# Kernel optimization log

Hardware: AMD Instinct MI355X
Metric: run time of the kernel (lower is better)

Reference implementation:

```python
import jax, jax.numpy as jnp
import numpy as np

B, Q, K, D, U = 8, 128, 512, 256, 256  # batch, q_len, kv_len, feat dim, units
NEG_INF = -1e6


def setup_inputs() -> dict:
    key = jax.random.key(0)
    ks = jax.random.split(key, 7)
    query = jax.random.normal(ks[0], (B, Q, D), dtype=jnp.float32)
    k_in = jax.random.normal(ks[1], (B, K, D), dtype=jnp.float32)
    value = jax.random.normal(ks[2], (B, K, D), dtype=jnp.float32)
    valid_len = jax.random.randint(ks[3], (B,), 1, K + 1, dtype=jnp.int32)
    s = 1.0 / np.sqrt(D)
    Wq = jax.random.uniform(ks[4], (D, U), jnp.float32, -s, s)
    Wk = jax.random.uniform(ks[5], (D, U), jnp.float32, -s, s)
    v_w = jax.random.uniform(ks[6], (U,), jnp.float32, -1.0 / np.sqrt(U), 1.0 / np.sqrt(U))
    return {"query": query, "key": k_in, "value": value, "valid_len": valid_len,
            "Wq": Wq, "Wk": Wk, "v_w": v_w}


def reference(query, key, value, valid_len, Wq, Wk, v_w):
    # projections: [B,Q,U] and [B,K,U]
    q = jnp.einsum('bqd,du->bqu', query, Wq)
    k = jnp.einsum('bkd,du->bku', key, Wk)
    # additive features [B,Q,K,U] -> tanh -> reduce with v: scores [B,Q,K]
    feats = jnp.tanh(q[:, :, None, :] + k[:, None, :, :])
    scores = jnp.einsum('bqku,u->bqk', feats, v_w)
    # masked softmax over keys: positions >= valid_len[b] masked out
    mask = jnp.arange(K)[None, None, :] < valid_len[:, None, None]
    scores = jnp.where(mask, scores, NEG_INF)
    attn = jax.nn.softmax(scores, axis=-1)
    # dropout p=0.0 (eval) -> identity
    return jnp.einsum('bqk,bkd->bqd', attn, value)
```

## Files before the change

### kernel.cpp

```cpp
#include <hip/hip_runtime.h>
#include <hip/hip_fp16.h>

#ifndef __has_builtin
#define __has_builtin(x) 0
#endif

__device__ __forceinline__ float fast_exp2(float x) {
#if __has_builtin(__builtin_amdgcn_exp2f)
  return __builtin_amdgcn_exp2f(x);
#else
  return exp2f(x);
#endif
}
__device__ __forceinline__ float fast_rcp(float x) {
#if __has_builtin(__builtin_amdgcn_rcpf)
  return __builtin_amdgcn_rcpf(x);
#else
  return 1.0f / x;
#endif
}

constexpr int Bsz = 8, QL = 128, KL = 512, DD = 256, UU = 256;
constexpr float NEG_INF = -1e6f;
constexpr float C2 = 2.885390081777927f;

typedef __attribute__((ext_vector_type(8))) short bf16x8;
typedef __attribute__((ext_vector_type(4))) float f32x4;

__device__ __forceinline__ ushort f2bf(float x) {
  uint u = __float_as_uint(x);
  u += 0x7FFFu + ((u >> 16) & 1u);
  return (ushort)(u >> 16);
}
__device__ __forceinline__ float bf2f(ushort h) {
  return __uint_as_float(((uint)h) << 16);
}

__device__ ushort g_wpk[2][2][16][8][64][8];

__global__ __launch_bounds__(256) void wpack_kernel(
    const float* __restrict__ Wq, const float* __restrict__ Wk)
{
  const int tid = blockIdx.x * 256 + threadIdx.x;
  const int src = tid >> 13;
  const int ut  = (tid >> 9) & 15;
  const int ks  = (tid >> 6) & 7;
  const int l   = tid & 63;
  const int u   = ut * 16 + (l & 15);
  const int d0  = ks * 32 + (l >> 4) * 8;
  const float* __restrict__ W = src ? Wk : Wq;

  ushort hi[8], lo[8];
#pragma unroll
  for (int j = 0; j < 8; ++j) {
    const float x = W[(size_t)(d0 + j) * UU + u];
    const ushort h = f2bf(x);
    hi[j] = h;
    lo[j] = f2bf(x - bf2f(h));
  }
#pragma unroll
  for (int j = 0; j < 8; ++j) g_wpk[src][0][ut][ks][l][j] = hi[j];
#pragma unroll
  for (int j = 0; j < 8; ++j) g_wpk[src][1][ut][ks][l][j] = lo[j];
}

__global__ __launch_bounds__(256) void proj_mfma_kernel(
    const float* __restrict__ query, const float* __restrict__ key,
    const int* __restrict__ valid_len,
    float* __restrict__ qp, __half* __restrict__ kpT)
{
  const int t = threadIdx.x, w = t >> 6, l = t & 63;
  const int blk = blockIdx.x;
  const bool isQ = blk < 64;

  int b = 0, k0 = 0, row_mem;
  if (isQ) {
    row_mem = blk * 16;
  } else {
    const int kt = blk - 64;
    b  = kt >> 5;
    k0 = (kt & 31) * 16;
    if (k0 >= valid_len[b]) return;
    row_mem = b * KL + k0;
  }
  const float* __restrict__ in = isQ ? query : key;
  const int src = isQ ? 0 : 1;

  bf16x8 Ah[8], Al[8];
  {
    const float* __restrict__ arow =
        in + (size_t)(row_mem + (l & 15)) * DD + ((l >> 4) * 8);
#pragma unroll
    for (int s = 0; s < 8; ++s) {
      const float4 x0 = *reinterpret_cast<const float4*>(arow + s * 32);
      const float4 x1 = *reinterpret_cast<const float4*>(arow + s * 32 + 4);
      const float v[8] = {x0.x, x0.y, x0.z, x0.w, x1.x, x1.y, x1.z, x1.w};
#pragma unroll
      for (int j = 0; j < 8; ++j) {
        const ushort h = f2bf(v[j]);
        Ah[s][j] = (short)h;
        Al[s][j] = (short)f2bf(v[j] - bf2f(h));
      }
    }
  }

  const int ut0 = w * 4;
#pragma unroll
  for (int tt = 0; tt < 4; ++tt) {
    const int ut = ut0 + tt;
    f32x4 acc = {0.f, 0.f, 0.f, 0.f};
#pragma unroll
    for (int s = 0; s < 8; ++s) {
      const bf16x8 bh = *reinterpret_cast<const bf16x8*>(&g_wpk[src][0][ut][s][l][0]);
      const bf16x8 bl = *reinterpret_cast<const bf16x8*>(&g_wpk[src][1][ut][s][l][0]);
      acc = __builtin_amdgcn_mfma_f32_16x16x32_bf16(Ah[s], bh, acc, 0, 0, 0);
      acc = __builtin_amdgcn_mfma_f32_16x16x32_bf16(Al[s], bh, acc, 0, 0, 0);
      acc = __builtin_amdgcn_mfma_f32_16x16x32_bf16(Ah[s], bl, acc, 0, 0, 0);
    }
    const int u  = ut * 16 + (l & 15);
    const int r4 = (l >> 4) * 4;
    if (isQ) {
      float* __restrict__ o = qp + (size_t)(row_mem + r4) * UU + u;
      o[0]          = fast_exp2(C2 * acc[0]);
      o[UU]         = fast_exp2(C2 * acc[1]);
      o[2 * UU]     = fast_exp2(C2 * acc[2]);
      o[3 * UU]     = fast_exp2(C2 * acc[3]);
    } else {
      ushort4 v;
      v.x = __half_as_ushort(__float2half_rn(fast_exp2(C2 * acc[0])));
      v.y = __half_as_ushort(__float2half_rn(fast_exp2(C2 * acc[1])));
      v.z = __half_as_ushort(__float2half_rn(fast_exp2(C2 * acc[2])));
      v.w = __half_as_ushort(__float2half_rn(fast_exp2(C2 * acc[3])));
      *reinterpret_cast<ushort4*>(
          kpT + ((size_t)(b * UU) + u) * KL + k0 + r4) = v;
    }
  }
}

__global__ __launch_bounds__(512) void fused_attn_kernel(
    const float* __restrict__ value, const int* __restrict__ valid_len,
    const float* __restrict__ v_w, const float* __restrict__ qp,
    const __half* __restrict__ kpT, float* __restrict__ out)
{
  __shared__ __align__(16) float4 qpack[UU];
  __shared__ __align__(16) float2 sp_part[8][8][64];
  __shared__ __align__(16) float  sps0[KL];
  __shared__ __align__(16) float  sps1[KL];
  __shared__ __align__(16) float2 opart[DD];
  __shared__ float2 redM[8], redS[8];

  const int t = threadIdx.x;
  const int w = t >> 6, l = t & 63;

  const int g = blockIdx.x;
  const int x = g & 7;
  const int i = g >> 3;
  int vl[8];
#pragma unroll
  for (int bi = 0; bi < 8; ++bi) vl[bi] = valid_len[bi];
  const int rk = (i < 32) ? x : (7 - x);
  int b = 0;
#pragma unroll
  for (int bi = 0; bi < 8; ++bi) {
    int r = 0;
#pragma unroll
    for (int bj = 0; bj < 8; ++bj)
      r += (vl[bj] > vl[bi]) || (vl[bj] == vl[bi] && bj < bi);
    if (r == rk) b = bi;
  }
  const int vlen = vl[b];
  const int q0 = i * 2;
  const int nc = (vlen + 63) >> 6;

  if (t < UU) {
    qpack[t] = make_float4(qp[(size_t)(b * QL + q0) * UU + t],
                           qp[(size_t)(b * QL + q0 + 1) * UU + t],
                           v_w[t], 0.f);
  }
  __syncthreads();

  {
    const __half* __restrict__ kbase =
        kpT + ((size_t)(b * UU) + 32 * w) * KL + l;
    for (int c = 0; c < nc; ++c) {
      const int k64 = 64 * c;
      float a0 = 0.f, a1 = 0.f;
      float cb[8], nb[8];
#pragma unroll
      for (int j = 0; j < 8; ++j)
        cb[j] = __half2float(kbase[(size_t)j * KL + k64]);
#pragma unroll 1
      for (int ug = 0; ug < 32; ug += 8) {
        const int un = (ug + 8 < 32) ? ug + 8 : 0;
#pragma unroll
        for (int j = 0; j < 8; ++j)
          nb[j] = __half2float(kbase[(size_t)(un + j) * KL + k64]);
#pragma unroll
        for (int j = 0; j < 8; j += 2) {
          const float4 qv0 = qpack[32 * w + ug + j];
          const float4 qv1 = qpack[32 * w + ug + j + 1];
          const float d00 = fmaf(qv0.x, cb[j],     1.0f);
          const float d01 = fmaf(qv1.x, cb[j + 1], 1.0f);
          const float num0 = fmaf(qv0.z, d01, qv1.z * d00);
          a0 = fmaf(num0, fast_rcp(d00 * d01), a0);
          const float d10 = fmaf(qv0.y, cb[j],     1.0f);
          const float d11 = fmaf(qv1.y, cb[j + 1], 1.0f);
          const float num1 = fmaf(qv0.z, d11, qv1.z * d10);
          a1 = fmaf(num1, fast_rcp(d10 * d11), a1);
        }
#pragma unroll
        for (int j = 0; j < 8; ++j) cb[j] = nb[j];
      }
      sp_part[w][c][l] = make_float2(a0, a1);
    }
  }
  __syncthreads();

  float s0 = 0.f, s1 = 0.f;
#pragma unroll
  for (int ws = 0; ws < 8; ++ws) {
    const float2 p = sp_part[ws][w][l];
    s0 += p.x; s1 += p.y;
  }
  const int key = t;
  s0 = (key < vlen) ? -(s0 + s0) : NEG_INF;
  s1 = (key < vlen) ? -(s1 + s1) : NEG_INF;

  float mx0 = s0, mx1 = s1;
#pragma unroll
  for (int off = 32; off >= 1; off >>= 1) {
    mx0 = fmaxf(mx0, __shfl_xor(mx0, off, 64));
    mx1 = fmaxf(mx1, __shfl_xor(mx1, off, 64));
  }
  if (l == 0) redM[w] = make_float2(mx0, mx1);
  __syncthreads();
  float m0 = redM[0].x, m1 = redM[0].y;
#pragma unroll
  for (int j = 1; j < 8; ++j) {
    m0 = fmaxf(m0, redM[j].x);
    m1 = fmaxf(m1, redM[j].y);
  }

  const float e0 = __expf(s0 - m0);
  const float e1 = __expf(s1 - m1);
  sps0[key] = e0;
  sps1[key] = e1;
  float ss0 = e0, ss1 = e1;
#pragma unroll
  for (int off = 32; off >= 1; off >>= 1) {
    ss0 += __shfl_xor(ss0, off, 64);
    ss1 += __shfl_xor(ss1, off, 64);
  }
  if (l == 0) redS[w] = make_float2(ss0, ss1);
  __syncthreads();
  float sum0 = redS[0].x, sum1 = redS[0].y;
#pragma unroll
  for (int j = 1; j < 8; ++j) {
    sum0 += redS[j].x;
    sum1 += redS[j].y;
  }
  const float inv0 = fast_rcp(sum0);
  const float inv1 = fast_rcp(sum1);

  const int h = t >> 8, d = t & 255;
  const int kmax  = (vlen + 15) & ~15;
  const int khalf = ((kmax >> 1) + 15) & ~15;
  const int kst = h ? khalf : 0;
  const int ken = h ? kmax : khalf;

  float o0 = 0.f, o1 = 0.f;
  if (ken > kst) {
    const float* __restrict__ vb = value + (size_t)b * KL * DD + d;
    float vc[16], vn[16];
#pragma unroll
    for (int j = 0; j < 16; ++j) vc[j] = vb[(size_t)(kst + j) * DD];
#pragma unroll 1
    for (int k = kst; k < ken; k += 16) {
      const int kn = (k + 16 < ken) ? k + 16 : kst;
#pragma unroll
      for (int j = 0; j < 16; ++j) vn[j] = vb[(size_t)(kn + j) * DD];
      const float4* __restrict__ p4 = reinterpret_cast<const float4*>(sps0 + k);
      const float4* __restrict__ q4 = reinterpret_cast<const float4*>(sps1 + k);
      const float4 p0 = p4[0], p1 = p4[1], p2 = p4[2], p3 = p4[3];
      const float4 r0 = q4[0], r1 = q4[1], r2 = q4[2], r3 = q4[3];
      o0 = fmaf(p0.x, vc[0],  o0); o1 = fmaf(r0.x, vc[0],  o1);
      o0 = fmaf(p0.y, vc[1],  o0); o1 = fmaf(r0.y, vc[1],  o1);
      o0 = fmaf(p0.z, vc[2],  o0); o1 = fmaf(r0.z, vc[2],  o1);
      o0 = fmaf(p0.w, vc[3],  o0); o1 = fmaf(r0.w, vc[3],  o1);
      o0 = fmaf(p1.x, vc[4],  o0); o1 = fmaf(r1.x, vc[4],  o1);
      o0 = fmaf(p1.y, vc[5],  o0); o1 = fmaf(r1.y, vc[5],  o1);
      o0 = fmaf(p1.z, vc[6],  o0); o1 = fmaf(r1.z, vc[6],  o1);
      o0 = fmaf(p1.w, vc[7],  o0); o1 = fmaf(r1.w, vc[7],  o1);
      o0 = fmaf(p2.x, vc[8],  o0); o1 = fmaf(r2.x, vc[8],  o1);
      o0 = fmaf(p2.y, vc[9],  o0); o1 = fmaf(r2.y, vc[9],  o1);
      o0 = fmaf(p2.z, vc[10], o0); o1 = fmaf(r2.z, vc[10], o1);
      o0 = fmaf(p2.w, vc[11], o0); o1 = fmaf(r2.w, vc[11], o1);
      o0 = fmaf(p3.x, vc[12], o0); o1 = fmaf(r3.x, vc[12], o1);
      o0 = fmaf(p3.y, vc[13], o0); o1 = fmaf(r3.y, vc[13], o1);
      o0 = fmaf(p3.z, vc[14], o0); o1 = fmaf(r3.z, vc[14], o1);
      o0 = fmaf(p3.w, vc[15], o0); o1 = fmaf(r3.w, vc[15], o1);
#pragma unroll
      for (int j = 0; j < 16; ++j) vc[j] = vn[j];
    }
  }
  if (h) opart[d] = make_float2(o0, o1);
  __syncthreads();
  if (!h) {
    const float2 p = opart[d];
    out[(size_t)(b * QL + q0) * DD + d]     = (o0 + p.x) * inv0;
    out[(size_t)(b * QL + q0 + 1) * DD + d] = (o1 + p.y) * inv1;
  }
}

extern "C" void kernel_launch(void* const* d_in, const int* in_sizes, int n_in,
                              void* d_out, int out_size, void* d_ws, size_t ws_size,
                              hipStream_t stream) {
  const float* query     = (const float*)d_in[0];
  const float* key       = (const float*)d_in[1];
  const float* value     = (const float*)d_in[2];
  const int*   valid_len = (const int*)d_in[3];
  const float* Wq        = (const float*)d_in[4];
  const float* Wk        = (const float*)d_in[5];
  const float* v_w       = (const float*)d_in[6];
  float* out = (float*)d_out;

  float*  qp  = (float*)d_ws;
  __half* kpT = (__half*)(qp + (size_t)Bsz * QL * UU);

  wpack_kernel<<<64, 256, 0, stream>>>(Wq, Wk);

  const int proj_blocks = 64 + 256;
  proj_mfma_kernel<<<proj_blocks, 256, 0, stream>>>(query, key, valid_len,
                                                    qp, kpT);

  const int fused_blocks = Bsz * QL / 2;
  fused_attn_kernel<<<fused_blocks, 512, 0, stream>>>(value, valid_len, v_w,
                                                      qp, kpT, out);
}
```

Before: 106.0 us.

## Interleave K projection in u-pairs and vectorize value accumulation across waves

The projection kernel now writes the exponentiated K projection as interleaved half2 pairs of adjacent units, so the score loop loads 32-bit words and converts two units at once. It also prefetches the next 64-key chunk across the whole chunk instead of per unit group. The attention-times-value stage changes from two half-blocks of scalar per-d loads to each wave taking strided 16-key groups and each lane reading a float4 of d, followed by an 8-way shared-memory reduction. This aims to widen global loads and balance key work across all waves, at the cost of more shared memory and a larger final reduction.

```diff
diff --git a/kernel.cpp b/kernel.cpp
--- a/kernel.cpp
+++ b/kernel.cpp
@@ -126,13 +126,12 @@
       o[2 * UU]     = fast_exp2(C2 * acc[2]);
       o[3 * UU]     = fast_exp2(C2 * acc[3]);
     } else {
-      ushort4 v;
-      v.x = __half_as_ushort(__float2half_rn(fast_exp2(C2 * acc[0])));
-      v.y = __half_as_ushort(__float2half_rn(fast_exp2(C2 * acc[1])));
-      v.z = __half_as_ushort(__float2half_rn(fast_exp2(C2 * acc[2])));
-      v.w = __half_as_ushort(__float2half_rn(fast_exp2(C2 * acc[3])));
-      *reinterpret_cast<ushort4*>(
-          kpT + ((size_t)(b * UU) + u) * KL + k0 + r4) = v;
+      __half* __restrict__ base =
+          kpT + (((size_t)b * 128 + (u >> 1)) * KL + (k0 + r4)) * 2 + (u & 1);
+      base[0] = __float2half_rn(fast_exp2(C2 * acc[0]));
+      base[2] = __float2half_rn(fast_exp2(C2 * acc[1]));
+      base[4] = __float2half_rn(fast_exp2(C2 * acc[2]));
+      base[6] = __float2half_rn(fast_exp2(C2 * acc[3]));
     }
   }
 }
@@ -146,7 +145,8 @@
   __shared__ __align__(16) float2 sp_part[8][8][64];
   __shared__ __align__(16) float  sps0[KL];
   __shared__ __align__(16) float  sps1[KL];
-  __shared__ __align__(16) float2 opart[DD];
+  __shared__ __align__(16) float  opA[8][DD];
+  __shared__ __align__(16) float  opB[8][DD];
   __shared__ float2 redM[8], redS[8];
 
   const int t = threadIdx.x;
@@ -180,38 +180,45 @@
   __syncthreads();
 
   {
-    const __half* __restrict__ kbase =
-        kpT + ((size_t)(b * UU) + 32 * w) * KL + l;
+    const uint* __restrict__ kb32 =
+        reinterpret_cast<const uint*>(kpT) + ((size_t)b * 128 + 16 * w) * KL + l;
+    uint cu[8], nu[8];
+#pragma unroll
+    for (int j = 0; j < 8; ++j) cu[j] = kb32[(size_t)j * KL];
+#pragma unroll
+    for (int j = 0; j < 8; ++j) nu[j] = kb32[(size_t)(8 + j) * KL];
+
     for (int c = 0; c < nc; ++c) {
-      const int k64 = 64 * c;
+      const int kn64 = (c + 1 < nc) ? 64 * (c + 1) : 0;
+      uint pu[8], pn[8];
+#pragma unroll
+      for (int j = 0; j < 8; ++j) pu[j] = kb32[(size_t)j * KL + kn64];
+#pragma unroll
+      for (int j = 0; j < 8; ++j) pn[j] = kb32[(size_t)(8 + j) * KL + kn64];
+
       float a0 = 0.f, a1 = 0.f;
-      float cb[8], nb[8];
-#pragma unroll
-      for (int j = 0; j < 8; ++j)
-        cb[j] = __half2float(kbase[(size_t)j * KL + k64]);
-#pragma unroll 1
-      for (int ug = 0; ug < 32; ug += 8) {
-        const int un = (ug + 8 < 32) ? ug + 8 : 0;
-#pragma unroll
-        for (int j = 0; j < 8; ++j)
-          nb[j] = __half2float(kbase[(size_t)(un + j) * KL + k64]);
-#pragma unroll
-        for (int j = 0; j < 8; j += 2) {
-          const float4 qv0 = qpack[32 * w + ug + j];
-          const float4 qv1 = qpack[32 * w + ug + j + 1];
-          const float d00 = fmaf(qv0.x, cb[j],     1.0f);
-          const float d01 = fmaf(qv1.x, cb[j + 1], 1.0f);
+#pragma unroll
+      for (int grp = 0; grp < 2; ++grp) {
+#pragma unroll
+        for (int j = 0; j < 8; ++j) {
+          const int upl = grp * 8 + j;
+          const uint pv = grp ? nu[j] : cu[j];
+          const float2 ek = __half22float2(*reinterpret_cast<const __half2*>(&pv));
+          const float4 qv0 = qpack[32 * w + 2 * upl];
+          const float4 qv1 = qpack[32 * w + 2 * upl + 1];
+          const float d00 = fmaf(qv0.x, ek.x, 1.0f);
+          const float d01 = fmaf(qv1.x, ek.y, 1.0f);
           const float num0 = fmaf(qv0.z, d01, qv1.z * d00);
           a0 = fmaf(num0, fast_rcp(d00 * d01), a0);
-          const float d10 = fmaf(qv0.y, cb[j],     1.0f);
-          const float d11 = fmaf(qv1.y, cb[j + 1], 1.0f);
+          const float d10 = fmaf(qv0.y, ek.x, 1.0f);
+          const float d11 = fmaf(qv1.y, ek.y, 1.0f);
           const float num1 = fmaf(qv0.z, d11, qv1.z * d10);
           a1 = fmaf(num1, fast_rcp(d10 * d11), a1);
         }
-#pragma unroll
-        for (int j = 0; j < 8; ++j) cb[j] = nb[j];
       }
       sp_part[w][c][l] = make_float2(a0, a1);
+#pragma unroll
+      for (int j = 0; j < 8; ++j) { cu[j] = pu[j]; nu[j] = pn[j]; }
     }
   }
   __syncthreads();
@@ -262,53 +269,51 @@
   const float inv0 = fast_rcp(sum0);
   const float inv1 = fast_rcp(sum1);
 
-  const int h = t >> 8, d = t & 255;
-  const int kmax  = (vlen + 15) & ~15;
-  const int khalf = ((kmax >> 1) + 15) & ~15;
-  const int kst = h ? khalf : 0;
-  const int ken = h ? kmax : khalf;
-
-  float o0 = 0.f, o1 = 0.f;
-  if (ken > kst) {
-    const float* __restrict__ vb = value + (size_t)b * KL * DD + d;
-    float vc[16], vn[16];
-#pragma unroll
-    for (int j = 0; j < 16; ++j) vc[j] = vb[(size_t)(kst + j) * DD];
+  const int dg = l;
+  const int kgroups = ((vlen + 15) & ~15) >> 4;
+  const float4* __restrict__ vb4 =
+      reinterpret_cast<const float4*>(value + (size_t)b * KL * DD) + dg;
+
+  float4 o0 = {0.f, 0.f, 0.f, 0.f}, o1 = {0.f, 0.f, 0.f, 0.f};
 #pragma unroll 1
-    for (int k = kst; k < ken; k += 16) {
-      const int kn = (k + 16 < ken) ? k + 16 : kst;
-#pragma unroll
-      for (int j = 0; j < 16; ++j) vn[j] = vb[(size_t)(kn + j) * DD];
-      const float4* __restrict__ p4 = reinterpret_cast<const float4*>(sps0 + k);
-      const float4* __restrict__ q4 = reinterpret_cast<const float4*>(sps1 + k);
-      const float4 p0 = p4[0], p1 = p4[1], p2 = p4[2], p3 = p4[3];
-      const float4 r0 = q4[0], r1 = q4[1], r2 = q4[2], r3 = q4[3];
-      o0 = fmaf(p0.x, vc[0],  o0); o1 = fmaf(r0.x, vc[0],  o1);
-      o0 = fmaf(p0.y, vc[1],  o0); o1 = fmaf(r0.y, vc[1],  o1);
-      o0 = fmaf(p0.z, vc[2],  o0); o1 = fmaf(r0.z, vc[2],  o1);
-      o0 = fmaf(p0.w, vc[3],  o0); o1 = fmaf(r0.w, vc[3],  o1);
-      o0 = fmaf(p1.x, vc[4],  o0); o1 = fmaf(r1.x, vc[4],  o1);
-      o0 = fmaf(p1.y, vc[5],  o0); o1 = fmaf(r1.y, vc[5],  o1);
-      o0 = fmaf(p1.z, vc[6],  o0); o1 = fmaf(r1.z, vc[6],  o1);
-      o0 = fmaf(p1.w, vc[7],  o0); o1 = fmaf(r1.w, vc[7],  o1);
-      o0 = fmaf(p2.x, vc[8],  o0); o1 = fmaf(r2.x, vc[8],  o1);
-      o0 = fmaf(p2.y, vc[9],  o0); o1 = fmaf(r2.y, vc[9],  o1);
-      o0 = fmaf(p2.z, vc[10], o0); o1 = fmaf(r2.z, vc[10], o1);
-      o0 = fmaf(p2.w, vc[11], o0); o1 = fmaf(r2.w, vc[11], o1);
-      o0 = fmaf(p3.x, vc[12], o0); o1 = fmaf(r3.x, vc[12], o1);
-      o0 = fmaf(p3.y, vc[13], o0); o1 = fmaf(r3.y, vc[13], o1);
-      o0 = fmaf(p3.z, vc[14], o0); o1 = fmaf(r3.z, vc[14], o1);
-      o0 = fmaf(p3.w, vc[15], o0); o1 = fmaf(r3.w, vc[15], o1);
-#pragma unroll
-      for (int j = 0; j < 16; ++j) vc[j] = vn[j];
-    }
-  }
-  if (h) opart[d] = make_float2(o0, o1);
-  __syncthreads();
-  if (!h) {
-    const float2 p = opart[d];
-    out[(size_t)(b * QL + q0) * DD + d]     = (o0 + p.x) * inv0;
-    out[(size_t)(b * QL + q0 + 1) * DD + d] = (o1 + p.y) * inv1;
+  for (int gg = w; gg < kgroups; gg += 8) {
+    const int k = gg * 16;
+#pragma unroll
+    for (int jj = 0; jj < 16; jj += 4) {
+      const float4 p0 = *reinterpret_cast<const float4*>(&sps0[k + jj]);
+      const float4 p1 = *reinterpret_cast<const float4*>(&sps1[k + jj]);
+      const float4 v0 = vb4[(size_t)(k + jj) * 64];
+      const float4 v1 = vb4[(size_t)(k + jj + 1) * 64];
+      const float4 v2 = vb4[(size_t)(k + jj + 2) * 64];
+      const float4 v3 = vb4[(size_t)(k + jj + 3) * 64];
+      o0.x = fmaf(p0.x, v0.x, o0.x); o0.y = fmaf(p0.x, v0.y, o0.y);
+      o0.z = fmaf(p0.x, v0.z, o0.z); o0.w = fmaf(p0.x, v0.w, o0.w);
+      o1.x = fmaf(p1.x, v0.x, o1.x); o1.y = fmaf(p1.x, v0.y, o1.y);
+      o1.z = fmaf(p1.x, v0.z, o1.z); o1.w = fmaf(p1.x, v0.w, o1.w);
+      o0.x = fmaf(p0.y, v1.x, o0.x); o0.y = fmaf(p0.y, v1.y, o0.y);
+      o0.z = fmaf(p0.y, v1.z, o0.z); o0.w = fmaf(p0.y, v1.w, o0.w);
+      o1.x = fmaf(p1.y, v1.x, o1.x); o1.y = fmaf(p1.y, v1.y, o1.y);
+      o1.z = fmaf(p1.y, v1.z, o1.z); o1.w = fmaf(p1.y, v1.w, o1.w);
+      o0.x = fmaf(p0.z, v2.x, o0.x); o0.y = fmaf(p0.z, v2.y, o0.y);
+      o0.z = fmaf(p0.z, v2.z, o0.z); o0.w = fmaf(p0.z, v2.w, o0.w);
+      o1.x = fmaf(p1.z, v2.x, o1.x); o1.y = fmaf(p1.z, v2.y, o1.y);
+      o1.z = fmaf(p1.z, v2.z, o1.z); o1.w = fmaf(p1.z, v2.w, o1.w);
+      o0.x = fmaf(p0.w, v3.x, o0.x); o0.y = fmaf(p0.w, v3.y, o0.y);
+      o0.z = fmaf(p0.w, v3.z, o0.z); o0.w = fmaf(p0.w, v3.w, o0.w);
+      o1.x = fmaf(p1.w, v3.x, o1.x); o1.y = fmaf(p1.w, v3.y, o1.y);
+      o1.z = fmaf(p1.w, v3.z, o1.z); o1.w = fmaf(p1.w, v3.w, o1.w);
+    }
+  }
+  *reinterpret_cast<float4*>(&opA[w][4 * dg]) = o0;
+  *reinterpret_cast<float4*>(&opB[w][4 * dg]) = o1;
+  __syncthreads();
+
+  if (t < DD) {
+    float a = 0.f, c = 0.f;
+#pragma unroll
+    for (int s = 0; s < 8; ++s) { a += opA[s][t]; c += opB[s][t]; }
+    out[(size_t)(b * QL + q0) * DD + t]     = a * inv0;
+    out[(size_t)(b * QL + q0 + 1) * DD + t] = c * inv1;
   }
 }
 
```

Measured after the change: 103.4 us. 2.5% less time.
